# Kernel optimization log

Hardware: AMD Instinct MI355X
Metric: run time of the kernel (lower is better)

## Reference

```python
import jax, jax.numpy as jnp
import numpy as np


def _sq_dist(q, k):
    # pairwise squared L2 distance: [B,H,L,D] x [B,H,M,D] -> [B,H,L,M]
    q2 = jnp.sum(q * q, axis=-1)[..., :, None]
    k2 = jnp.sum(k * k, axis=-1)[..., None, :]
    qk = jnp.einsum('bhld,bhmd->bhlm', q, k)
    return q2 + k2 - 2.0 * qk


def setup_inputs() -> dict:
    key = jax.random.key(0)
    k1, k2, k3 = jax.random.split(key, 3)
    B, H, L, D = 2, 8, 2048, 64
    query = jax.random.normal(k1, (B, H, L, D), dtype=jnp.float32)
    key_t = jax.random.normal(k2, (B, H, L, D), dtype=jnp.float32)
    mask = jnp.ones((B, L), dtype=jnp.float32)
    # mu param: normal(0, 0.5) * [0,1][:,None,None] -> first component zeroed
    mu = (jax.random.normal(k3, (2, H, D), dtype=jnp.float32) * 0.5
          * jnp.array([0.0, 1.0], dtype=jnp.float32)[:, None, None])
    pi = jnp.array([0.5, 0.5], dtype=jnp.float32)
    return {'query': query, 'key': key_t, 'mask': mask, 'mu': mu, 'pi': pi}


def reference(query, key, mask, mu, pi):
    D = query.shape[-1]
    var = D ** 0.5  # self.var = head_dim ** 0.5
    neg = 1e6 * (1.0 - mask[:, None, None, :])  # [B,1,1,L]
    pic = jnp.clip(pi, 0.0, 1.0)
    qk1 = (-0.5 / var) * _sq_dist(query, key - mu[0][None, :, None, :]) - neg
    qk2 = (-0.5 / var) * _sq_dist(query, key - mu[1][None, :, None, :]) - neg
    attn = jnp.exp(qk1) * pic[0] + jnp.exp(qk2) * pic[1]
    return attn / jnp.sum(attn, axis=-1, keepdims=True)
```

## Files before the change

### kernel.cpp

```cpp
#include <hip/hip_runtime.h>
#include <math.h>

#define B_ 2
#define H_ 8
#define L_ 2048
#define D_ 64
#define BM 16
#define NT 256
#define NBLK 32
#define L2E 1.4426950408889634f

typedef _Float16 half8 __attribute__((ext_vector_type(8)));
typedef __attribute__((ext_vector_type(4))) float f4;

#define MFMA16F(a, b, c) __builtin_amdgcn_mfma_f32_16x16x32_f16(a, b, c, 0, 0, 0)

struct LdsT {
  float muv[2][D_];
  float er0[BM], er1[BM];
  float red[4][BM];
};

__device__ inline half8 cvt8(const float4& a0, const float4& a1) {
  half8 r;
  r[0] = (_Float16)a0.x; r[1] = (_Float16)a0.y;
  r[2] = (_Float16)a0.z; r[3] = (_Float16)a0.w;
  r[4] = (_Float16)a1.x; r[5] = (_Float16)a1.y;
  r[6] = (_Float16)a1.z; r[7] = (_Float16)a1.w;
  return r;
}

__global__ __launch_bounds__(256) void prep_kernel(
    const float* __restrict__ k, const float* __restrict__ mask,
    const float* __restrict__ mu, float2* __restrict__ ck,
    half8* __restrict__ wf)
{
  int u   = blockIdx.x * 256 + threadIdx.x;
  int col = u >> 3;
  int g   = u & 7;
  int bh  = col >> 11, c = col & 2047;
  int b   = bh >> 3,   h = bh & 7;
  const float s = -0.0625f;
  const float* kp  = k + (((size_t)bh * L_ + c) * D_) + 8 * g;
  const float* mu0 = mu + (size_t)h * D_ + 8 * g;
  const float* mu1 = mu + (size_t)(H_ * D_) + (size_t)h * D_ + 8 * g;
  float4 x0 = *reinterpret_cast<const float4*>(kp);
  float4 x1 = *reinterpret_cast<const float4*>(kp + 4);
  float xs[8] = {x0.x, x0.y, x0.z, x0.w, x1.x, x1.y, x1.z, x1.w};
  float s0 = 0.f, s1 = 0.f;
#pragma unroll
  for (int i = 0; i < 8; ++i) {
    float a;
    a = xs[i] - mu0[i]; s0 += a * a;
    a = xs[i] - mu1[i]; s1 += a * a;
  }
  s0 += __shfl_xor(s0, 1, 64); s0 += __shfl_xor(s0, 2, 64); s0 += __shfl_xor(s0, 4, 64);
  s1 += __shfl_xor(s1, 1, 64); s1 += __shfl_xor(s1, 2, 64); s1 += __shfl_xor(s1, 4, 64);
  if (g == 0) {
    float neg = 1.0e6f * (1.0f - mask[(size_t)b * L_ + c]);
    ck[(size_t)bh * L_ + c] = make_float2(exp2f((s * s0 - neg) * L2E),
                                          exp2f((s * s1 - neg) * L2E));
  }
  int blk = c >> 4, ci = c & 15;
  wf[((size_t)bh * 128 + blk) * 128 + (g >> 2) * 64 + (g & 3) * 16 + ci] =
      cvt8(x0, x1);
}

template <bool USE_WS>
__global__ __launch_bounds__(NT, 8) void mg_kernel(
    const float* __restrict__ q, const float* __restrict__ kk,
    const float* __restrict__ mask, const float* __restrict__ mu,
    const float* __restrict__ pi, const float2* __restrict__ ckw,
    const half8* __restrict__ wf, float* __restrict__ out)
{
  __shared__ LdsT S;
  const int t = threadIdx.x;
  int bid = blockIdx.x;
  int vwg = (bid & 7) * 256 + (bid >> 3);
  int bh  = vwg >> 7;
  int rb  = vwg & 127;
  int b = bh >> 3, h = bh & 7;
  int row0 = rb * BM;

  const int w  = t >> 6;
  const int ln = t & 63;
  const int ci = ln & 15;
  const int kg = ln >> 4;

  const float s   = -0.0625f;
  const float DDC = 0.125f * L2E;

  const float*  maskb = mask + (size_t)b * L_;
  const float2* ckb   = ckw + (size_t)bh * L_;
  const half8*  wfb   = wf + (size_t)bh * (128 * 128);

  if (t < 2 * D_)
    S.muv[t >> 6][t & 63] =
        mu[(size_t)(t >> 6) * (H_ * D_) + (size_t)h * D_ + (t & 63)];

  half8 ah[2];
  {
    const float* qrow = q + ((size_t)bh * L_ + row0 + ci) * D_;
#pragma unroll
    for (int h2 = 0; h2 < 2; ++h2) {
      float4 a0 = *reinterpret_cast<const float4*>(qrow + 32 * h2 + kg * 8);
      float4 a1 = *reinterpret_cast<const float4*>(qrow + 32 * h2 + kg * 8 + 4);
      ah[h2] = cvt8(a0, a1);
    }
  }
  __syncthreads();

  if (t < BM) {
    float pi0 = fminf(fmaxf(pi[0], 0.f), 1.f);
    float pi1 = fminf(fmaxf(pi[1], 0.f), 1.f);
    const float* qr = q + ((size_t)bh * L_ + row0 + t) * D_;
    float a0 = 0.f, a1 = 0.f, a2 = 0.f;
#pragma unroll
    for (int dq = 0; dq < 16; ++dq) {
      float4 qv = *reinterpret_cast<const float4*>(qr + 4 * dq);
      a0 += qv.x * qv.x + qv.y * qv.y + qv.z * qv.z + qv.w * qv.w;
      a1 += qv.x * S.muv[0][4*dq] + qv.y * S.muv[0][4*dq+1] +
            qv.z * S.muv[0][4*dq+2] + qv.w * S.muv[0][4*dq+3];
      a2 += qv.x * S.muv[1][4*dq] + qv.y * S.muv[1][4*dq+1] +
            qv.z * S.muv[1][4*dq+2] + qv.w * S.muv[1][4*dq+3];
    }
    S.er0[t] = pi0 * exp2f((s * a0 + 2.f * s * a1) * L2E);
    S.er1[t] = pi1 * exp2f((s * a0 + 2.f * s * a2) * L2E);
  }
  __syncthreads();

  float e0r[4], e1r[4];
#pragma unroll
  for (int reg = 0; reg < 4; ++reg) {
    e0r[reg] = S.er0[kg * 4 + reg];
    e1r[reg] = S.er1[kg * 4 + reg];
  }

  auto LOADCOL = [&](int blk, half8& b0, half8& b1, float2& ec) {
    if (USE_WS) {
      const half8* pb = wfb + (size_t)blk * 128;
      b0 = pb[ln];
      b1 = pb[64 + ln];
      ec = ckb[blk * 16 + ci];
    } else {
      int col = blk * 16 + ci;
      const float* kp = kk + ((size_t)bh * L_ + col) * D_;
      float4 x0 = *reinterpret_cast<const float4*>(kp + 8 * kg);
      float4 x1 = *reinterpret_cast<const float4*>(kp + 8 * kg + 4);
      float4 x2 = *reinterpret_cast<const float4*>(kp + 32 + 8 * kg);
      float4 x3 = *reinterpret_cast<const float4*>(kp + 32 + 8 * kg + 4);
      b0 = cvt8(x0, x1);
      b1 = cvt8(x2, x3);
      int d0 = 8 * kg, d1 = 32 + 8 * kg;
      float s0 = 0.f, s1 = 0.f;
      float xs[8] = {x0.x, x0.y, x0.z, x0.w, x1.x, x1.y, x1.z, x1.w};
      float ys[8] = {x2.x, x2.y, x2.z, x2.w, x3.x, x3.y, x3.z, x3.w};
#pragma unroll
      for (int i = 0; i < 8; ++i) {
        float a;
        a = xs[i] - S.muv[0][d0 + i]; s0 += a * a;
        a = xs[i] - S.muv[1][d0 + i]; s1 += a * a;
        a = ys[i] - S.muv[0][d1 + i]; s0 += a * a;
        a = ys[i] - S.muv[1][d1 + i]; s1 += a * a;
      }
      s0 += __shfl_xor(s0, 16, 64); s0 += __shfl_xor(s0, 32, 64);
      s1 += __shfl_xor(s1, 16, 64); s1 += __shfl_xor(s1, 32, 64);
      float neg = 1.0e6f * (1.0f - maskb[col]);
      ec = make_float2(exp2f((s * s0 - neg) * L2E),
                       exp2f((s * s1 - neg) * L2E));
    }
  };

  float rsum[4] = {0.f, 0.f, 0.f, 0.f};
  const int blkw = w * NBLK;
#pragma unroll 4
  for (int j = 0; j < NBLK; ++j) {
    half8 b0, b1; float2 ec;
    LOADCOL(blkw + j, b0, b1, ec);
    f4 acc = {0.f, 0.f, 0.f, 0.f};
    acc = MFMA16F(ah[0], b0, acc);
    acc = MFMA16F(ah[1], b1, acc);
#pragma unroll
    for (int reg = 0; reg < 4; ++reg) {
      float g2 = __builtin_amdgcn_exp2f(DDC * acc[reg]);
      float m  = fmaf(e0r[reg], ec.x, e1r[reg] * ec.y);
      rsum[reg] = fmaf(g2, m, rsum[reg]);
    }
  }

#pragma unroll
  for (int reg = 0; reg < 4; ++reg) {
    float v = rsum[reg];
    v += __shfl_xor(v, 1, 64);
    v += __shfl_xor(v, 2, 64);
    v += __shfl_xor(v, 4, 64);
    v += __shfl_xor(v, 8, 64);
    if (ci == 0) S.red[w][kg * 4 + reg] = v;
  }
  __syncthreads();
#pragma unroll
  for (int reg = 0; reg < 4; ++reg) {
    int r = kg * 4 + reg;
    float inv = 1.0f / (S.red[0][r] + S.red[1][r] + S.red[2][r] + S.red[3][r]);
    e0r[reg] *= inv;
    e1r[reg] *= inv;
  }

  float* ob = out + ((size_t)bh * L_ + row0 + kg * 4) * L_ + w * 512 + ci;
#pragma unroll 4
  for (int j = 0; j < NBLK; ++j) {
    half8 b0, b1; float2 ec;
    LOADCOL(blkw + j, b0, b1, ec);
    f4 acc = {0.f, 0.f, 0.f, 0.f};
    acc = MFMA16F(ah[0], b0, acc);
    acc = MFMA16F(ah[1], b1, acc);
#pragma unroll
    for (int reg = 0; reg < 4; ++reg) {
      float g2 = __builtin_amdgcn_exp2f(DDC * acc[reg]);
      float m  = fmaf(e0r[reg], ec.x, e1r[reg] * ec.y);
      float p  = g2 * m;
      __builtin_nontemporal_store(p, ob + (size_t)reg * L_ + j * 16);
    }
  }
}

extern "C" void kernel_launch(void* const* d_in, const int* in_sizes, int n_in,
                              void* d_out, int out_size, void* d_ws, size_t ws_size,
                              hipStream_t stream) {
  const float* q    = (const float*)d_in[0];
  const float* k    = (const float*)d_in[1];
  const float* mask = (const float*)d_in[2];
  const float* mu   = (const float*)d_in[3];
  const float* pi   = (const float*)d_in[4];
  float* out = (float*)d_out;

  const size_t ck_bytes = (size_t)B_ * H_ * L_ * sizeof(float2);
  const size_t wp_bytes = (size_t)B_ * H_ * L_ * D_ * sizeof(short);
  const bool use_ws = (ws_size >= ck_bytes + wp_bytes) && (d_ws != nullptr);

  if (use_ws) {
    float2* ck = (float2*)d_ws;
    half8*  wf = (half8*)((char*)d_ws + ck_bytes);
    prep_kernel<<<dim3(B_ * H_ * L_ * 8 / 256), dim3(256), 0, stream>>>(
        k, mask, mu, ck, wf);
    mg_kernel<true><<<dim3(B_ * H_ * (L_ / BM)), dim3(NT), 0, stream>>>(
        q, k, mask, mu, pi, ck, wf, out);
  } else {
    mg_kernel<false><<<dim3(B_ * H_ * (L_ / BM)), dim3(NT), 0, stream>>>(
        q, k, mask, mu, pi, nullptr, nullptr, out);
  }
}
```

Baseline: 98.65 us.

## Split fused row-sum and write passes into separate sum and write kernels

The fused kernel that computed row sums and then wrote normalized outputs is split into two launches: one computes per-row sums into a workspace buffer, the other recomputes the scores and writes them normalized. The intent is to decouple the compute-heavy sum phase from the store-heavy write phase so each kernel can schedule more uniformly. In exchange it adds a kernel launch, a second prologue, and an extra round-trip of row sums through global memory, and the workspace requirement grows.

Result: slower. 123.8 us (+25.5%).

```diff
diff --git a/kernel.cpp b/kernel.cpp
--- a/kernel.cpp
+++ b/kernel.cpp
@@ -66,12 +66,166 @@
       cvt8(x0, x1);
 }
 
-template <bool USE_WS>
-__global__ __launch_bounds__(NT, 8) void mg_kernel(
+__device__ inline void prologue(
+    LdsT& S, const float* q, const float* mu, const float* pi,
+    int bh, int h, int row0, int t, int ci, int kg,
+    half8 ah[2], float e0r[4], float e1r[4])
+{
+  const float s = -0.0625f;
+  if (t < 2 * D_)
+    S.muv[t >> 6][t & 63] =
+        mu[(size_t)(t >> 6) * (H_ * D_) + (size_t)h * D_ + (t & 63)];
+  {
+    const float* qrow = q + ((size_t)bh * L_ + row0 + ci) * D_;
+#pragma unroll
+    for (int h2 = 0; h2 < 2; ++h2) {
+      float4 a0 = *reinterpret_cast<const float4*>(qrow + 32 * h2 + kg * 8);
+      float4 a1 = *reinterpret_cast<const float4*>(qrow + 32 * h2 + kg * 8 + 4);
+      ah[h2] = cvt8(a0, a1);
+    }
+  }
+  __syncthreads();
+  if (t < BM) {
+    float pi0 = fminf(fmaxf(pi[0], 0.f), 1.f);
+    float pi1 = fminf(fmaxf(pi[1], 0.f), 1.f);
+    const float* qr = q + ((size_t)bh * L_ + row0 + t) * D_;
+    float a0 = 0.f, a1 = 0.f, a2 = 0.f;
+#pragma unroll
+    for (int dq = 0; dq < 16; ++dq) {
+      float4 qv = *reinterpret_cast<const float4*>(qr + 4 * dq);
+      a0 += qv.x * qv.x + qv.y * qv.y + qv.z * qv.z + qv.w * qv.w;
+      a1 += qv.x * S.muv[0][4*dq] + qv.y * S.muv[0][4*dq+1] +
+            qv.z * S.muv[0][4*dq+2] + qv.w * S.muv[0][4*dq+3];
+      a2 += qv.x * S.muv[1][4*dq] + qv.y * S.muv[1][4*dq+1] +
+            qv.z * S.muv[1][4*dq+2] + qv.w * S.muv[1][4*dq+3];
+    }
+    S.er0[t] = pi0 * exp2f((s * a0 + 2.f * s * a1) * L2E);
+    S.er1[t] = pi1 * exp2f((s * a0 + 2.f * s * a2) * L2E);
+  }
+  __syncthreads();
+#pragma unroll
+  for (int reg = 0; reg < 4; ++reg) {
+    e0r[reg] = S.er0[kg * 4 + reg];
+    e1r[reg] = S.er1[kg * 4 + reg];
+  }
+}
+
+__global__ __launch_bounds__(NT, 8) void sum_kernel(
+    const float* __restrict__ q, const float* __restrict__ mu,
+    const float* __restrict__ pi, const float2* __restrict__ ckw,
+    const half8* __restrict__ wf, float* __restrict__ rs)
+{
+  __shared__ LdsT S;
+  const int t = threadIdx.x;
+  int bid = blockIdx.x;
+  int vwg = (bid & 7) * 256 + (bid >> 3);
+  int bh  = vwg >> 7;
+  int rb  = vwg & 127;
+  int h = bh & 7;
+  int row0 = rb * BM;
+  const int w  = t >> 6;
+  const int ln = t & 63;
+  const int ci = ln & 15;
+  const int kg = ln >> 4;
+  const float DDC = 0.125f * L2E;
+
+  const float2* ckb = ckw + (size_t)bh * L_;
+  const half8*  wfb = wf + (size_t)bh * (128 * 128);
+
+  half8 ah[2]; float e0r[4], e1r[4];
+  prologue(S, q, mu, pi, bh, h, row0, t, ci, kg, ah, e0r, e1r);
+
+  float rsum[4] = {0.f, 0.f, 0.f, 0.f};
+  const int blkw = w * NBLK;
+#pragma unroll 4
+  for (int j = 0; j < NBLK; ++j) {
+    const half8* pb = wfb + (size_t)(blkw + j) * 128;
+    half8 b0 = pb[ln];
+    half8 b1 = pb[64 + ln];
+    float2 ec = ckb[(blkw + j) * 16 + ci];
+    f4 acc = {0.f, 0.f, 0.f, 0.f};
+    acc = MFMA16F(ah[0], b0, acc);
+    acc = MFMA16F(ah[1], b1, acc);
+#pragma unroll
+    for (int reg = 0; reg < 4; ++reg) {
+      float g2 = __builtin_amdgcn_exp2f(DDC * acc[reg]);
+      float m  = fmaf(e0r[reg], ec.x, e1r[reg] * ec.y);
+      rsum[reg] = fmaf(g2, m, rsum[reg]);
+    }
+  }
+#pragma unroll
+  for (int reg = 0; reg < 4; ++reg) {
+    float v = rsum[reg];
+    v += __shfl_xor(v, 1, 64);
+    v += __shfl_xor(v, 2, 64);
+    v += __shfl_xor(v, 4, 64);
+    v += __shfl_xor(v, 8, 64);
+    if (ci == 0) S.red[w][kg * 4 + reg] = v;
+  }
+  __syncthreads();
+  if (t < BM)
+    rs[(size_t)bh * L_ + row0 + t] =
+        S.red[0][t] + S.red[1][t] + S.red[2][t] + S.red[3][t];
+}
+
+__global__ __launch_bounds__(NT, 8) void write_kernel(
+    const float* __restrict__ q, const float* __restrict__ mu,
+    const float* __restrict__ pi, const float2* __restrict__ ckw,
+    const half8* __restrict__ wf, const float* __restrict__ rs,
+    float* __restrict__ out)
+{
+  __shared__ LdsT S;
+  const int t = threadIdx.x;
+  int bid = blockIdx.x;
+  int vwg = (bid & 7) * 256 + (bid >> 3);
+  int bh  = vwg >> 7;
+  int rb  = vwg & 127;
+  int h = bh & 7;
+  int row0 = rb * BM;
+  const int w  = t >> 6;
+  const int ln = t & 63;
+  const int ci = ln & 15;
+  const int kg = ln >> 4;
+  const float DDC = 0.125f * L2E;
+
+  const float2* ckb = ckw + (size_t)bh * L_;
+  const half8*  wfb = wf + (size_t)bh * (128 * 128);
+
+  half8 ah[2]; float e0r[4], e1r[4];
+  prologue(S, q, mu, pi, bh, h, row0, t, ci, kg, ah, e0r, e1r);
+
+#pragma unroll
+  for (int reg = 0; reg < 4; ++reg) {
+    float inv = 1.0f / rs[(size_t)bh * L_ + row0 + kg * 4 + reg];
+    e0r[reg] *= inv;
+    e1r[reg] *= inv;
+  }
+
+  const int blkw = w * NBLK;
+  float* ob = out + ((size_t)bh * L_ + row0 + kg * 4) * L_ + w * 512 + ci;
+#pragma unroll 4
+  for (int j = 0; j < NBLK; ++j) {
+    const half8* pb = wfb + (size_t)(blkw + j) * 128;
+    half8 b0 = pb[ln];
+    half8 b1 = pb[64 + ln];
+    float2 ec = ckb[(blkw + j) * 16 + ci];
+    f4 acc = {0.f, 0.f, 0.f, 0.f};
+    acc = MFMA16F(ah[0], b0, acc);
+    acc = MFMA16F(ah[1], b1, acc);
+#pragma unroll
+    for (int reg = 0; reg < 4; ++reg) {
+      float g2 = __builtin_amdgcn_exp2f(DDC * acc[reg]);
+      float m  = fmaf(e0r[reg], ec.x, e1r[reg] * ec.y);
+      float p  = g2 * m;
+      __builtin_nontemporal_store(p, ob + (size_t)reg * L_ + j * 16);
+    }
+  }
+}
+
+__global__ __launch_bounds__(NT, 8) void mg_fb_kernel(
     const float* __restrict__ q, const float* __restrict__ kk,
     const float* __restrict__ mask, const float* __restrict__ mu,
-    const float* __restrict__ pi, const float2* __restrict__ ckw,
-    const half8* __restrict__ wf, float* __restrict__ out)
+    const float* __restrict__ pi, float* __restrict__ out)
 {
   __shared__ LdsT S;
   const int t = threadIdx.x;
@@ -81,94 +235,41 @@
   int rb  = vwg & 127;
   int b = bh >> 3, h = bh & 7;
   int row0 = rb * BM;
-
   const int w  = t >> 6;
   const int ln = t & 63;
   const int ci = ln & 15;
   const int kg = ln >> 4;
-
-  const float s   = -0.0625f;
-  const float DDC = 0.125f * L2E;
-
-  const float*  maskb = mask + (size_t)b * L_;
-  const float2* ckb   = ckw + (size_t)bh * L_;
-  const half8*  wfb   = wf + (size_t)bh * (128 * 128);
-
-  if (t < 2 * D_)
-    S.muv[t >> 6][t & 63] =
-        mu[(size_t)(t >> 6) * (H_ * D_) + (size_t)h * D_ + (t & 63)];
-
-  half8 ah[2];
-  {
-    const float* qrow = q + ((size_t)bh * L_ + row0 + ci) * D_;
-#pragma unroll
-    for (int h2 = 0; h2 < 2; ++h2) {
-      float4 a0 = *reinterpret_cast<const float4*>(qrow + 32 * h2 + kg * 8);
-      float4 a1 = *reinterpret_cast<const float4*>(qrow + 32 * h2 + kg * 8 + 4);
-      ah[h2] = cvt8(a0, a1);
-    }
-  }
-  __syncthreads();
-
-  if (t < BM) {
-    float pi0 = fminf(fmaxf(pi[0], 0.f), 1.f);
-    float pi1 = fminf(fmaxf(pi[1], 0.f), 1.f);
-    const float* qr = q + ((size_t)bh * L_ + row0 + t) * D_;
-    float a0 = 0.f, a1 = 0.f, a2 = 0.f;
-#pragma unroll
-    for (int dq = 0; dq < 16; ++dq) {
-      float4 qv = *reinterpret_cast<const float4*>(qr + 4 * dq);
-      a0 += qv.x * qv.x + qv.y * qv.y + qv.z * qv.z + qv.w * qv.w;
-      a1 += qv.x * S.muv[0][4*dq] + qv.y * S.muv[0][4*dq+1] +
-            qv.z * S.muv[0][4*dq+2] + qv.w * S.muv[0][4*dq+3];
-      a2 += qv.x * S.muv[1][4*dq] + qv.y * S.muv[1][4*dq+1] +
-            qv.z * S.muv[1][4*dq+2] + qv.w * S.muv[1][4*dq+3];
-    }
-    S.er0[t] = pi0 * exp2f((s * a0 + 2.f * s * a1) * L2E);
-    S.er1[t] = pi1 * exp2f((s * a0 + 2.f * s * a2) * L2E);
-  }
-  __syncthreads();
-
-  float e0r[4], e1r[4];
-#pragma unroll
-  for (int reg = 0; reg < 4; ++reg) {
-    e0r[reg] = S.er0[kg * 4 + reg];
-    e1r[reg] = S.er1[kg * 4 + reg];
-  }
+  const float s = -0.0625f, DDC = 0.125f * L2E;
+  const float* maskb = mask + (size_t)b * L_;
+
+  half8 ah[2]; float e0r[4], e1r[4];
+  prologue(S, q, mu, pi, bh, h, row0, t, ci, kg, ah, e0r, e1r);
 
   auto LOADCOL = [&](int blk, half8& b0, half8& b1, float2& ec) {
-    if (USE_WS) {
-      const half8* pb = wfb + (size_t)blk * 128;
-      b0 = pb[ln];
-      b1 = pb[64 + ln];
-      ec = ckb[blk * 16 + ci];
-    } else {
-      int col = blk * 16 + ci;
-      const float* kp = kk + ((size_t)bh * L_ + col) * D_;
-      float4 x0 = *reinterpret_cast<const float4*>(kp + 8 * kg);
-      float4 x1 = *reinterpret_cast<const float4*>(kp + 8 * kg + 4);
-      float4 x2 = *reinterpret_cast<const float4*>(kp + 32 + 8 * kg);
-      float4 x3 = *reinterpret_cast<const float4*>(kp + 32 + 8 * kg + 4);
-      b0 = cvt8(x0, x1);
-      b1 = cvt8(x2, x3);
-      int d0 = 8 * kg, d1 = 32 + 8 * kg;
-      float s0 = 0.f, s1 = 0.f;
-      float xs[8] = {x0.x, x0.y, x0.z, x0.w, x1.x, x1.y, x1.z, x1.w};
-      float ys[8] = {x2.x, x2.y, x2.z, x2.w, x3.x, x3.y, x3.z, x3.w};
-#pragma unroll
-      for (int i = 0; i < 8; ++i) {
-        float a;
-        a = xs[i] - S.muv[0][d0 + i]; s0 += a * a;
-        a = xs[i] - S.muv[1][d0 + i]; s1 += a * a;
-        a = ys[i] - S.muv[0][d1 + i]; s0 += a * a;
-        a = ys[i] - S.muv[1][d1 + i]; s1 += a * a;
-      }
-      s0 += __shfl_xor(s0, 16, 64); s0 += __shfl_xor(s0, 32, 64);
-      s1 += __shfl_xor(s1, 16, 64); s1 += __shfl_xor(s1, 32, 64);
-      float neg = 1.0e6f * (1.0f - maskb[col]);
-      ec = make_float2(exp2f((s * s0 - neg) * L2E),
-                       exp2f((s * s1 - neg) * L2E));
-    }
+    int col = blk * 16 + ci;
+    const float* kp = kk + ((size_t)bh * L_ + col) * D_;
+    float4 x0 = *reinterpret_cast<const float4*>(kp + 8 * kg);
+    float4 x1 = *reinterpret_cast<const float4*>(kp + 8 * kg + 4);
+    float4 x2 = *reinterpret_cast<const float4*>(kp + 32 + 8 * kg);
+    float4 x3 = *reinterpret_cast<const float4*>(kp + 32 + 8 * kg + 4);
+    b0 = cvt8(x0, x1);
+    b1 = cvt8(x2, x3);
+    int d0 = 8 * kg, d1 = 32 + 8 * kg;
+    float s0 = 0.f, s1 = 0.f;
+    float xs[8] = {x0.x, x0.y, x0.z, x0.w, x1.x, x1.y, x1.z, x1.w};
+    float ys[8] = {x2.x, x2.y, x2.z, x2.w, x3.x, x3.y, x3.z, x3.w};
+#pragma unroll
+    for (int i = 0; i < 8; ++i) {
+      float a;
+      a = xs[i] - S.muv[0][d0 + i]; s0 += a * a;
+      a = xs[i] - S.muv[1][d0 + i]; s1 += a * a;
+      a = ys[i] - S.muv[0][d1 + i]; s0 += a * a;
+      a = ys[i] - S.muv[1][d1 + i]; s1 += a * a;
+    }
+    s0 += __shfl_xor(s0, 16, 64); s0 += __shfl_xor(s0, 32, 64);
+    s1 += __shfl_xor(s1, 16, 64); s1 += __shfl_xor(s1, 32, 64);
+    float neg = 1.0e6f * (1.0f - maskb[col]);
+    ec = make_float2(exp2f((s * s0 - neg) * L2E), exp2f((s * s1 - neg) * L2E));
   };
 
   float rsum[4] = {0.f, 0.f, 0.f, 0.f};
@@ -187,7 +288,6 @@
       rsum[reg] = fmaf(g2, m, rsum[reg]);
     }
   }
-
 #pragma unroll
   for (int reg = 0; reg < 4; ++reg) {
     float v = rsum[reg];
@@ -205,7 +305,6 @@
     e0r[reg] *= inv;
     e1r[reg] *= inv;
   }
-
   float* ob = out + ((size_t)bh * L_ + row0 + kg * 4) * L_ + w * 512 + ci;
 #pragma unroll 4
   for (int j = 0; j < NBLK; ++j) {
@@ -218,8 +317,7 @@
     for (int reg = 0; reg < 4; ++reg) {
       float g2 = __builtin_amdgcn_exp2f(DDC * acc[reg]);
       float m  = fmaf(e0r[reg], ec.x, e1r[reg] * ec.y);
-      float p  = g2 * m;
-      __builtin_nontemporal_store(p, ob + (size_t)reg * L_ + j * 16);
+      __builtin_nontemporal_store(g2 * m, ob + (size_t)reg * L_ + j * 16);
     }
   }
 }
@@ -236,17 +334,21 @@
 
   const size_t ck_bytes = (size_t)B_ * H_ * L_ * sizeof(float2);
   const size_t wp_bytes = (size_t)B_ * H_ * L_ * D_ * sizeof(short);
-  const bool use_ws = (ws_size >= ck_bytes + wp_bytes) && (d_ws != nullptr);
+  const size_t rs_bytes = (size_t)B_ * H_ * L_ * sizeof(float);
+  const bool use_ws = (ws_size >= ck_bytes + wp_bytes + rs_bytes) && (d_ws != nullptr);
 
   if (use_ws) {
     float2* ck = (float2*)d_ws;
     half8*  wf = (half8*)((char*)d_ws + ck_bytes);
+    float*  rs = (float*)((char*)d_ws + ck_bytes + wp_bytes);
     prep_kernel<<<dim3(B_ * H_ * L_ * 8 / 256), dim3(256), 0, stream>>>(
         k, mask, mu, ck, wf);
-    mg_kernel<true><<<dim3(B_ * H_ * (L_ / BM)), dim3(NT), 0, stream>>>(
-        q, k, mask, mu, pi, ck, wf, out);
+    sum_kernel<<<dim3(B_ * H_ * (L_ / BM)), dim3(NT), 0, stream>>>(
+        q, mu, pi, ck, wf, rs);
+    write_kernel<<<dim3(B_ * H_ * (L_ / BM)), dim3(NT), 0, stream>>>(
+        q, mu, pi, ck, wf, rs, out);
   } else {
-    mg_kernel<false><<<dim3(B_ * H_ * (L_ / BM)), dim3(NT), 0, stream>>>(
-        q, k, mask, mu, pi, nullptr, nullptr, out);
-  }
-}
+    mg_fb_kernel<<<dim3(B_ * H_ * (L_ / BM)), dim3(NT), 0, stream>>>(
+        q, k, mask, mu, pi, out);
+  }
+}
```
